# Performance work log

Hardware: AMD Instinct MI355X
Metric: run time of the kernel (lower is better)

## Reference

```python
import jax, jax.numpy as jnp
import numpy as np

N_NODES = 100000


def _gcn_conv(x, row, col, W, b, n):
    # PyG GCNConv: h = W x; out_i = sum_{j->i} norm_ij * h_j + b, with self-loops
    # and symmetric normalization norm_ij = deg_i^-1/2 * deg_j^-1/2.
    h = x @ W  # [N, out]
    loop = jnp.arange(n, dtype=row.dtype)
    r = jnp.concatenate([row, loop])
    c = jnp.concatenate([col, loop])
    deg = jax.ops.segment_sum(jnp.ones_like(c, dtype=h.dtype), c, num_segments=n)
    dinv = jnp.where(deg > 0, jax.lax.rsqrt(deg), 0.0)
    norm = dinv[r] * dinv[c]  # [E+N]
    msg = h[r] * norm[:, None]  # gather + per-edge scale
    out = jax.ops.segment_sum(msg, c, num_segments=n)  # scatter-add to dst
    return out + b


def setup_inputs() -> dict:
    key = jax.random.key(0)
    ks = jax.random.split(key, 8)
    N, E = N_NODES, 1600000
    d_in, comm_dim, hid, out = 120, 8, 128, 64
    x = jax.random.normal(ks[0], (N, d_in), dtype=jnp.float32)
    edge_index = jax.random.randint(ks[1], (2, E), 0, N, dtype=jnp.int64)
    comm_ids = jax.random.randint(ks[2], (N,), 0, 64, dtype=jnp.int64)
    comm_emb = jax.random.normal(ks[3], (64, comm_dim), dtype=jnp.float32)
    s1 = 1.0 / np.sqrt(d_in + comm_dim)
    s2 = 1.0 / np.sqrt(hid)
    W1 = jax.random.normal(ks[4], (d_in + comm_dim, hid), dtype=jnp.float32) * s1
    b1 = jnp.zeros((hid,), dtype=jnp.float32)
    W2 = jax.random.normal(ks[5], (hid, out), dtype=jnp.float32) * s2
    b2 = jnp.zeros((out,), dtype=jnp.float32)
    return {"x": x, "edge_index": edge_index, "comm_ids": comm_ids,
            "comm_emb": comm_emb, "W1": W1, "b1": b1, "W2": W2, "b2": b2}


def reference(x, edge_index, comm_ids, comm_emb, W1, b1, W2, b2):
    n = x.shape[0]
    row, col = edge_index[0], edge_index[1]
    c = comm_emb[comm_ids]                      # [N, comm_dim] embedding lookup
    h = jnp.concatenate([x, c], axis=-1)        # [N, in+comm_dim]
    h = jax.nn.relu(_gcn_conv(h, row, col, W1, b1, n))
    # dropout p=0.5 is inactive in eval mode (training=False)
    out = _gcn_conv(h, row, col, W2, b2, n)     # [N, out_channels]
    return out
```

## Files before the change

### kernel.cpp

```cpp
#include <hip/hip_runtime.h>

typedef __attribute__((ext_vector_type(8))) short bf16x8;
typedef __attribute__((ext_vector_type(4))) float f32x4;

#define CAPB 5632
#define NBMAX 512

static __device__ __forceinline__ unsigned short f2bf(float f) {
    unsigned u = __float_as_uint(f);
    unsigned r = (u + 0x7fff + ((u >> 16) & 1)) >> 16;
    return (unsigned short)r;
}
static __device__ __forceinline__ float bfu_lo(unsigned v) { return __uint_as_float(v << 16); }
static __device__ __forceinline__ float bfu_hi(unsigned v) { return __uint_as_float(v & 0xffff0000u); }

static __device__ __forceinline__ bf16x8 cvt8(float4 u0, float4 u1) {
    bf16x8 r;
    r[0] = (short)f2bf(u0.x); r[1] = (short)f2bf(u0.y);
    r[2] = (short)f2bf(u0.z); r[3] = (short)f2bf(u0.w);
    r[4] = (short)f2bf(u1.x); r[5] = (short)f2bf(u1.y);
    r[6] = (short)f2bf(u1.z); r[7] = (short)f2bf(u1.w);
    return r;
}

__global__ void k_zero_int(int* __restrict__ p, int n) {
    int i = blockIdx.x * blockDim.x + threadIdx.x;
    if (i < n) p[i] = 0;
}

__global__ __launch_bounds__(256) void k_passA(const int* __restrict__ row,
                                               const int* __restrict__ col,
                                               int* __restrict__ gcnt,
                                               unsigned* __restrict__ packed,
                                               int E, int NB) {
    __shared__ int lcnt[NBMAX];
    __shared__ int lbase[NBMAX];
    __shared__ int lcur[NBMAX];
    __shared__ int gbaseS[NBMAX];
    __shared__ unsigned stage[4096];
    __shared__ unsigned short stageb[4096];
    __shared__ int s[256];

    int tid = threadIdx.x;
    int t0 = blockIdx.x * 4096;
    int total = min(4096, E - t0);

    for (int b = tid; b < NBMAX; b += 256) { lcnt[b] = 0; lcur[b] = 0; }
    __syncthreads();

    int er[16], ec[16];
#pragma unroll
    for (int j = 0; j < 16; ++j) {
        int e = t0 + j * 256 + tid;
        if (e < E) {
            er[j] = row[e];
            ec[j] = col[e];
            atomicAdd(&lcnt[ec[j] >> 8], 1);
        }
    }
    __syncthreads();

    int c0 = lcnt[2 * tid], c1 = lcnt[2 * tid + 1];
    int p = c0 + c1;
    s[tid] = p;
    __syncthreads();
    for (int off = 1; off < 256; off <<= 1) {
        int t = (tid >= off) ? s[tid - off] : 0;
        __syncthreads();
        s[tid] += t;
        __syncthreads();
    }
    int ebase = s[tid] - p;
    lbase[2 * tid] = ebase;
    lbase[2 * tid + 1] = ebase + c0;
    __syncthreads();

    for (int b = tid; b < NB; b += 256) {
        int lc = lcnt[b];
        if (lc > 0) gbaseS[b] = atomicAdd(&gcnt[b], lc);
    }
    __syncthreads();

#pragma unroll
    for (int j = 0; j < 16; ++j) {
        int e = t0 + j * 256 + tid;
        if (e < E) {
            int b = ec[j] >> 8;
            int pos = lbase[b] + atomicAdd(&lcur[b], 1);
            stage[pos] = ((unsigned)er[j] << 8) | ((unsigned)ec[j] & 255u);
            stageb[pos] = (unsigned short)b;
        }
    }
    __syncthreads();

    for (int j = tid; j < total; j += 256) {
        int b = stageb[j];
        packed[(size_t)b * CAPB + gbaseS[b] + (j - lbase[b])] = stage[j];
    }
}

__global__ void k_bscan(const int* __restrict__ gcnt, int* __restrict__ gbase,
                        int* __restrict__ indptr, int n, int E, int NB) {
    __shared__ int s[512];
    int tid = threadIdx.x;
    int v = (tid < NB) ? gcnt[tid] : 0;
    s[tid] = v;
    __syncthreads();
    for (int off = 1; off < 512; off <<= 1) {
        int t = (tid >= off) ? s[tid - off] : 0;
        __syncthreads();
        s[tid] += t;
        __syncthreads();
    }
    if (tid < NB) gbase[tid] = s[tid] - v;
    if (tid == 0) indptr[n] = E;
}

__global__ __launch_bounds__(256) void k_passB(const unsigned* __restrict__ packed,
                                               const int* __restrict__ gcnt,
                                               const int* __restrict__ gbase,
                                               int* __restrict__ indptr,
                                               float* __restrict__ dinv,
                                               int* __restrict__ srcidx, int n) {
    __shared__ int ncnt[256];
    __shared__ int nbase[256];
    __shared__ int srow[CAPB];

    int b = blockIdx.x;
    int tid = threadIdx.x;
    int nodeBase = b << 8;
    int cntE = min(gcnt[b], CAPB);
    int base = gbase[b];
    size_t pb = (size_t)b * CAPB;

    ncnt[tid] = 0;
    __syncthreads();

    for (int j = tid; j < cntE; j += 256) {
        unsigned e = packed[pb + j];
        atomicAdd(&ncnt[e & 255u], 1);
    }
    __syncthreads();

    int v = ncnt[tid];
    nbase[tid] = v;
    __syncthreads();
    for (int off = 1; off < 256; off <<= 1) {
        int t = (tid >= off) ? nbase[tid - off] : 0;
        __syncthreads();
        nbase[tid] += t;
        __syncthreads();
    }
    int excl = nbase[tid] - v;
    __syncthreads();
    nbase[tid] = excl;

    int node = nodeBase + tid;
    if (node < n) {
        indptr[node] = base + excl;
        dinv[node] = rsqrtf((float)(v + 1));
    }
    ncnt[tid] = 0;
    __syncthreads();

    for (int j = tid; j < cntE; j += 256) {
        unsigned e = packed[pb + j];
        int c = (int)(e & 255u);
        int r = (int)(e >> 8);
        int p = nbase[c] + atomicAdd(&ncnt[c], 1);
        srow[p] = r;
    }
    __syncthreads();

    for (int j = tid; j < cntE; j += 256) srcidx[base + j] = srow[j];
}

__global__ void k_wprep(const float* __restrict__ W1, const float* __restrict__ W2,
                        const float* __restrict__ b1,
                        unsigned short* __restrict__ Wt1, unsigned short* __restrict__ Wt2p,
                        float* __restrict__ b1p,
                        unsigned* __restrict__ D1qz,
                        unsigned* __restrict__ D2z,
                        unsigned char* __restrict__ shifts, int n) {
    int idx = blockIdx.x * blockDim.x + threadIdx.x;
    const int B0 = 128 * 128, B1 = B0 + 64 * 128, B2 = B1 + 128, B3 = B2 + 32, B4 = B3 + 32;
    if (idx < B0) {
        int colc = idx >> 7, k = idx & 127;
        Wt1[colc * 128 + k] = f2bf(W1[k * 128 + colc]);
    } else if (idx < B1) {
        int j = idx - B0;
        int colc = j >> 7, p = j & 127;
        int korig = (p & 7) * 16 + (p >> 3);
        Wt2p[colc * 128 + p] = f2bf(W2[korig * 64 + colc]);
    } else if (idx < B2) {
        int p = idx - B1;
        b1p[p] = b1[(p & 7) * 16 + (p >> 3)];
    } else if (idx < B3) {
        D1qz[idx - B2] = 0;
    } else if (idx < B4) {
        D2z[idx - B3] = 0;
    } else if (idx == B4) {
        shifts[n] = 0;
    }
}

__global__ __launch_bounds__(256) void k_gemm1(const float* __restrict__ x,
                                               const int* __restrict__ cid,
                                               const float* __restrict__ cemb,
                                               const unsigned short* __restrict__ Wt,
                                               const float* __restrict__ dinv,
                                               unsigned char* __restrict__ D1q,
                                               unsigned char* __restrict__ shifts, int n) {
    int tid = threadIdx.x;
    int wid = tid >> 6, lane = tid & 63;
    int rbase = blockIdx.x * 64 + wid * 16;
    int lr = lane & 15, kq = lane >> 4;

    int arow = rbase + lr;
    if (arow > n - 1) arow = n - 1;
    const float* xp = x + (size_t)arow * 120 + kq * 8;

    bf16x8 a0 = cvt8(*(const float4*)(xp),      *(const float4*)(xp + 4));
    bf16x8 a1 = cvt8(*(const float4*)(xp + 32), *(const float4*)(xp + 36));
    bf16x8 a2 = cvt8(*(const float4*)(xp + 64), *(const float4*)(xp + 68));
    bf16x8 a3;
    if (kq < 3) {
        a3 = cvt8(*(const float4*)(xp + 96), *(const float4*)(xp + 100));
    } else {
        const float* cp = cemb + (size_t)cid[arow] * 8;
        a3 = cvt8(*(const float4*)(cp), *(const float4*)(cp + 4));
    }

    f32x4 acc[8];
#pragma unroll
    for (int cf = 0; cf < 8; ++cf) acc[cf] = (f32x4){0.f, 0.f, 0.f, 0.f};

#pragma unroll
    for (int cf = 0; cf < 8; ++cf) {
        const unsigned short* bp = Wt + (size_t)(cf * 16 + lr) * 128 + kq * 8;
        bf16x8 b0 = *(const bf16x8*)(bp);
        bf16x8 b1 = *(const bf16x8*)(bp + 32);
        bf16x8 b2 = *(const bf16x8*)(bp + 64);
        bf16x8 b3 = *(const bf16x8*)(bp + 96);
        acc[cf] = __builtin_amdgcn_mfma_f32_16x16x32_bf16(a0, b0, acc[cf], 0, 0, 0);
        acc[cf] = __builtin_amdgcn_mfma_f32_16x16x32_bf16(a1, b1, acc[cf], 0, 0, 0);
        acc[cf] = __builtin_amdgcn_mfma_f32_16x16x32_bf16(a2, b2, acc[cf], 0, 0, 0);
        acc[cf] = __builtin_amdgcn_mfma_f32_16x16x32_bf16(a3, b3, acc[cf], 0, 0, 0);
    }

#pragma unroll
    for (int r = 0; r < 4; ++r) {
        int grow = rbase + kq * 4 + r;
        float dv = (grow < n) ? dinv[grow] : 0.f;
        float m = 0.f;
#pragma unroll
        for (int cf = 0; cf < 8; ++cf) m = fmaxf(m, fabsf(acc[cf][r] * dv));
        m = fmaxf(m, __shfl_xor(m, 1));
        m = fmaxf(m, __shfl_xor(m, 2));
        m = fmaxf(m, __shfl_xor(m, 4));
        m = fmaxf(m, __shfl_xor(m, 8));
        int mb = (int)((__float_as_uint(m) >> 23) & 255u);
        int er = mb - 127 + 1 - 7;
        int sh = min(max(er + 16, 0), 15);
        int ee = sh - 16;
        float sinv = __uint_as_float((unsigned)(127 - ee) << 23);
        if (grow < n) {
            if (lr == 0) shifts[grow] = (unsigned char)sh;
            unsigned lo = 0, hi = 0;
#pragma unroll
            for (int cf = 0; cf < 4; ++cf) {
                int q8 = (int)rintf(acc[cf][r] * dv * sinv);
                q8 = min(max(q8, -127), 127);
                lo |= ((unsigned)(q8 & 255)) << (8 * cf);
            }
#pragma unroll
            for (int cf = 4; cf < 8; ++cf) {
                int q8 = (int)rintf(acc[cf][r] * dv * sinv);
                q8 = min(max(q8, -127), 127);
                hi |= ((unsigned)(q8 & 255)) << (8 * (cf - 4));
            }
            *(uint2*)&D1q[(size_t)grow * 128 + lr * 8] = make_uint2(lo, hi);
        }
    }
}

__global__ __launch_bounds__(256) void k_agg1g2(const uint2* __restrict__ rows,
                                                const unsigned char* __restrict__ shifts,
                                                const int* __restrict__ indptr,
                                                const int* __restrict__ srcidx,
                                                const float* __restrict__ dinv,
                                                const float* __restrict__ b1p,
                                                const unsigned short* __restrict__ Wt2p,
                                                unsigned short* __restrict__ D2, int n) {
    __shared__ unsigned short Hl[16][132];
    int tid = threadIdx.x;
    int wid = tid >> 6, lane = tid & 63;
    int g = lane >> 4, gl = lane & 15;
    int i = blockIdx.x * 16 + wid * 4 + g;
    if (i > n - 1) i = n - 1;

    float di = dinv[i];
    float4 bA = *(const float4*)&b1p[gl * 8];
    float4 bB = *(const float4*)&b1p[gl * 8 + 4];

    uint2 sq = rows[(size_t)i * 16 + gl];
    int ssh = shifts[i];
    int a[8];
#pragma unroll
    for (int j = 0; j < 4; ++j) {
        a[j]     = ((int)(signed char)((sq.x >> (8 * j)) & 255u)) << ssh;
        a[j + 4] = ((int)(signed char)((sq.y >> (8 * j)) & 255u)) << ssh;
    }

    int e0 = indptr[i];
    int d = indptr[i + 1] - e0;
    int m = max(d, __shfl_xor(d, 16));
    m = max(m, __shfl_xor(m, 32));

#pragma unroll 8
    for (int t = 0; t < m; ++t) {
        bool act = t < d;
        int s = act ? srcidx[e0 + t] : n;
        int sh = shifts[s];
        uint2 q = rows[(size_t)s * 16 + gl];
#pragma unroll
        for (int j = 0; j < 4; ++j) {
            a[j]     += ((int)(signed char)((q.x >> (8 * j)) & 255u)) << sh;
            a[j + 4] += ((int)(signed char)((q.y >> (8 * j)) & 255u)) << sh;
        }
    }

    float sc = di * 0x1p-16f;
    int trow = wid * 4 + g;
    float hb[8] = {bA.x, bA.y, bA.z, bA.w, bB.x, bB.y, bB.z, bB.w};
#pragma unroll
    for (int j = 0; j < 8; ++j) {
        Hl[trow][gl * 8 + j] = f2bf(fmaxf((float)a[j] * sc + hb[j], 0.f));
    }
    __syncthreads();

    int lr = lane & 15, kq = lane >> 4;
    f32x4 acc = (f32x4){0.f, 0.f, 0.f, 0.f};
    const unsigned short* bp = Wt2p + (size_t)(wid * 16 + lr) * 128 + kq * 8;
#pragma unroll
    for (int step = 0; step < 4; ++step) {
        bf16x8 af = *(const bf16x8*)&Hl[lr][kq * 8 + step * 32];
        bf16x8 bf = *(const bf16x8*)(bp + step * 32);
        acc = __builtin_amdgcn_mfma_f32_16x16x32_bf16(af, bf, acc, 0, 0, 0);
    }
#pragma unroll
    for (int r = 0; r < 4; ++r) {
        int node = blockIdx.x * 16 + kq * 4 + r;
        if (node < n) {
            D2[(size_t)node * 64 + wid * 16 + lr] = f2bf(acc[r] * dinv[node]);
        }
    }
}

__global__ __launch_bounds__(256) void k_agg2(const uint2* __restrict__ Hs,
                                              const int* __restrict__ indptr,
                                              const int* __restrict__ srcidx,
                                              const float* __restrict__ dinv,
                                              const float* __restrict__ bias,
                                              float4* __restrict__ Out, int n) {
    int tid = threadIdx.x;
    int lane = tid & 63;
    int g = lane >> 4, gl = lane & 15;
    int i = blockIdx.x * 16 + (tid >> 6) * 4 + g;
    if (i > n - 1) i = n - 1;

    float di = dinv[i];
    float4 b = *(const float4*)&bias[gl * 4];

    uint2 sv = Hs[(size_t)i * 16 + gl];
    float a0 = bfu_lo(sv.x), a1 = bfu_hi(sv.x);
    float a2 = bfu_lo(sv.y), a3 = bfu_hi(sv.y);

    int e0 = indptr[i];
    int d = indptr[i + 1] - e0;
    int m = max(d, __shfl_xor(d, 16));
    m = max(m, __shfl_xor(m, 32));

#pragma unroll 8
    for (int t = 0; t < m; ++t) {
        bool act = t < d;
        int s = act ? srcidx[e0 + t] : n;
        uint2 w = Hs[(size_t)s * 16 + gl];
        a0 += bfu_lo(w.x);
        a1 += bfu_hi(w.x);
        a2 += bfu_lo(w.y);
        a3 += bfu_hi(w.y);
    }
    Out[(size_t)i * 16 + gl] = make_float4(di * a0 + b.x, di * a1 + b.y,
                                           di * a2 + b.z, di * a3 + b.w);
}


extern "C" void kernel_launch(void* const* d_in, const int* in_sizes, int n_in,
                              void* d_out, int out_size, void* d_ws, size_t ws_size,
                              hipStream_t stream) {
    const float* x    = (const float*)d_in[0];
    const int*   eidx = (const int*)d_in[1];
    const int*   cid  = (const int*)d_in[2];
    const float* cemb = (const float*)d_in[3];
    const float* W1   = (const float*)d_in[4];
    const float* b1   = (const float*)d_in[5];
    const float* W2   = (const float*)d_in[6];
    const float* b2   = (const float*)d_in[7];
    float* out = (float*)d_out;

    int n = in_sizes[2];
    int E = in_sizes[1] / 2;
    const int* row = eidx;
    const int* col = eidx + E;
    int NB = (n + 255) / 256;

    char* ws = (char*)d_ws;
    auto alloc = [&](size_t bytes) {
        char* p = ws;
        ws += (bytes + 255) & ~(size_t)255;
        return p;
    };
    float*          dinv    = (float*)alloc((size_t)n * 4);
    int*            gcnt    = (int*)alloc((size_t)NB * 4);
    int*            gbase   = (int*)alloc((size_t)NB * 4);
    int*            indptr  = (int*)alloc((size_t)(n + 1) * 4);
    int*            srcidx  = (int*)alloc((size_t)E * 4);
    unsigned*       packed  = (unsigned*)alloc((size_t)NB * CAPB * 4);
    unsigned short* Wt1     = (unsigned short*)alloc(128 * 128 * 2);
    unsigned short* Wt2p    = (unsigned short*)alloc(64 * 128 * 2);
    float*          b1p     = (float*)alloc(128 * 4);
    unsigned char*  D1q     = (unsigned char*)alloc((size_t)(n + 1) * 128);
    unsigned char*  shifts  = (unsigned char*)alloc((size_t)(n + 1));
    unsigned short* D2      = (unsigned short*)alloc((size_t)(n + 1) * 64 * 2);

    k_zero_int<<<(NB + 255) / 256, 256, 0, stream>>>(gcnt, NB);
    k_passA<<<(E + 4095) / 4096, 256, 0, stream>>>(row, col, gcnt, packed, E, NB);
    k_bscan<<<1, 512, 0, stream>>>(gcnt, gbase, indptr, n, E, NB);
    k_passB<<<NB, 256, 0, stream>>>(packed, gcnt, gbase, indptr, dinv, srcidx, n);

    int wpn = 128 * 128 + 64 * 128 + 128 + 32 + 32 + 1;
    k_wprep<<<(wpn + 255) / 256, 256, 0, stream>>>(
        W1, W2, b1, Wt1, Wt2p, b1p,
        (unsigned*)(D1q + (size_t)n * 128),
        (unsigned*)(D2 + (size_t)n * 64),
        shifts, n);

    int gb = (n + 63) / 64;
    int ga = (n + 15) / 16;
    k_gemm1<<<gb, 256, 0, stream>>>(x, cid, cemb, Wt1, dinv, D1q, shifts, n);
    k_agg1g2<<<ga, 256, 0, stream>>>((const uint2*)D1q, shifts, indptr, srcidx,
                                     dinv, b1p, Wt2p, D2, n);
    k_agg2<<<ga, 256, 0, stream>>>((const uint2*)D2, indptr, srcidx, dinv, b2,
                                   (float4*)out, n);
}
```

Before: 188.5 us.

## Give each wave 16 nodes in agg1g2 and drop block-wide sync before MFMA

```diff
diff --git a/kernel.cpp b/kernel.cpp
--- a/kernel.cpp
+++ b/kernel.cpp
@@ -13,6 +13,9 @@
 }
 static __device__ __forceinline__ float bfu_lo(unsigned v) { return __uint_as_float(v << 16); }
 static __device__ __forceinline__ float bfu_hi(unsigned v) { return __uint_as_float(v & 0xffff0000u); }
+static __device__ __forceinline__ unsigned packbf(float a, float b) {
+    return (unsigned)f2bf(a) | ((unsigned)f2bf(b) << 16);
+}
 
 static __device__ __forceinline__ bf16x8 cvt8(float4 u0, float4 u1) {
     bf16x8 r;
@@ -180,10 +183,9 @@
                         unsigned short* __restrict__ Wt1, unsigned short* __restrict__ Wt2p,
                         float* __restrict__ b1p,
                         unsigned* __restrict__ D1qz,
-                        unsigned* __restrict__ D2z,
                         unsigned char* __restrict__ shifts, int n) {
     int idx = blockIdx.x * blockDim.x + threadIdx.x;
-    const int B0 = 128 * 128, B1 = B0 + 64 * 128, B2 = B1 + 128, B3 = B2 + 32, B4 = B3 + 32;
+    const int B0 = 128 * 128, B1 = B0 + 64 * 128, B2 = B1 + 128, B3 = B2 + 32;
     if (idx < B0) {
         int colc = idx >> 7, k = idx & 127;
         Wt1[colc * 128 + k] = f2bf(W1[k * 128 + colc]);
@@ -197,11 +199,13 @@
         b1p[p] = b1[(p & 7) * 16 + (p >> 3)];
     } else if (idx < B3) {
         D1qz[idx - B2] = 0;
-    } else if (idx < B4) {
-        D2z[idx - B3] = 0;
-    } else if (idx == B4) {
+    } else if (idx == B3) {
         shifts[n] = 0;
     }
+}
+
+__global__ void k_zrow(unsigned* __restrict__ D2z) {
+    if (threadIdx.x < 32) D2z[threadIdx.x] = 0;
 }
 
 __global__ __launch_bounds__(256) void k_gemm1(const float* __restrict__ x,
@@ -292,67 +296,84 @@
                                                 const float* __restrict__ b1p,
                                                 const unsigned short* __restrict__ Wt2p,
                                                 unsigned short* __restrict__ D2, int n) {
-    __shared__ unsigned short Hl[16][132];
+    __shared__ unsigned short Hl[4][16][132];
     int tid = threadIdx.x;
     int wid = tid >> 6, lane = tid & 63;
     int g = lane >> 4, gl = lane & 15;
-    int i = blockIdx.x * 16 + wid * 4 + g;
-    if (i > n - 1) i = n - 1;
-
-    float di = dinv[i];
+    int nbase = blockIdx.x * 64 + wid * 16;
+
     float4 bA = *(const float4*)&b1p[gl * 8];
     float4 bB = *(const float4*)&b1p[gl * 8 + 4];
-
-    uint2 sq = rows[(size_t)i * 16 + gl];
-    int ssh = shifts[i];
-    int a[8];
-#pragma unroll
-    for (int j = 0; j < 4; ++j) {
-        a[j]     = ((int)(signed char)((sq.x >> (8 * j)) & 255u)) << ssh;
-        a[j + 4] = ((int)(signed char)((sq.y >> (8 * j)) & 255u)) << ssh;
-    }
-
-    int e0 = indptr[i];
-    int d = indptr[i + 1] - e0;
-    int m = max(d, __shfl_xor(d, 16));
-    m = max(m, __shfl_xor(m, 32));
+    float hb[8] = {bA.x, bA.y, bA.z, bA.w, bB.x, bB.y, bB.z, bB.w};
+
+#pragma unroll
+    for (int b = 0; b < 4; ++b) {
+        int i = nbase + b * 4 + g;
+        if (i > n - 1) i = n - 1;
+        float di = dinv[i];
+
+        uint2 sq = rows[(size_t)i * 16 + gl];
+        int ssh = shifts[i];
+        int a[8];
+#pragma unroll
+        for (int j = 0; j < 4; ++j) {
+            a[j]     = ((int)(signed char)((sq.x >> (8 * j)) & 255u)) << ssh;
+            a[j + 4] = ((int)(signed char)((sq.y >> (8 * j)) & 255u)) << ssh;
+        }
+
+        int e0 = indptr[i];
+        int d = indptr[i + 1] - e0;
+        int m = max(d, __shfl_xor(d, 16));
+        m = max(m, __shfl_xor(m, 32));
 
 #pragma unroll 8
-    for (int t = 0; t < m; ++t) {
-        bool act = t < d;
-        int s = act ? srcidx[e0 + t] : n;
-        int sh = shifts[s];
-        uint2 q = rows[(size_t)s * 16 + gl];
-#pragma unroll
-        for (int j = 0; j < 4; ++j) {
-            a[j]     += ((int)(signed char)((q.x >> (8 * j)) & 255u)) << sh;
-            a[j + 4] += ((int)(signed char)((q.y >> (8 * j)) & 255u)) << sh;
-        }
-    }
-
-    float sc = di * 0x1p-16f;
-    int trow = wid * 4 + g;
-    float hb[8] = {bA.x, bA.y, bA.z, bA.w, bB.x, bB.y, bB.z, bB.w};
-#pragma unroll
-    for (int j = 0; j < 8; ++j) {
-        Hl[trow][gl * 8 + j] = f2bf(fmaxf((float)a[j] * sc + hb[j], 0.f));
-    }
-    __syncthreads();
+        for (int t = 0; t < m; ++t) {
+            bool act = t < d;
+            int s = act ? srcidx[e0 + t] : n;
+            int sh = shifts[s];
+            uint2 q = rows[(size_t)s * 16 + gl];
+#pragma unroll
+            for (int j = 0; j < 4; ++j) {
+                a[j]     += ((int)(signed char)((q.x >> (8 * j)) & 255u)) << sh;
+                a[j + 4] += ((int)(signed char)((q.y >> (8 * j)) & 255u)) << sh;
+            }
+        }
+
+        float sc = di * 0x1p-16f;
+        uint4 o;
+        o.x = packbf(fmaxf((float)a[0] * sc + hb[0], 0.f), fmaxf((float)a[1] * sc + hb[1], 0.f));
+        o.y = packbf(fmaxf((float)a[2] * sc + hb[2], 0.f), fmaxf((float)a[3] * sc + hb[3], 0.f));
+        o.z = packbf(fmaxf((float)a[4] * sc + hb[4], 0.f), fmaxf((float)a[5] * sc + hb[5], 0.f));
+        o.w = packbf(fmaxf((float)a[6] * sc + hb[6], 0.f), fmaxf((float)a[7] * sc + hb[7], 0.f));
+        *(uint4*)&Hl[wid][b * 4 + g][gl * 8] = o;
+    }
+
+    asm volatile("s_waitcnt lgkmcnt(0)" ::: "memory");
+    __builtin_amdgcn_sched_barrier(0);
 
     int lr = lane & 15, kq = lane >> 4;
-    f32x4 acc = (f32x4){0.f, 0.f, 0.f, 0.f};
-    const unsigned short* bp = Wt2p + (size_t)(wid * 16 + lr) * 128 + kq * 8;
-#pragma unroll
-    for (int step = 0; step < 4; ++step) {
-        bf16x8 af = *(const bf16x8*)&Hl[lr][kq * 8 + step * 32];
-        bf16x8 bf = *(const bf16x8*)(bp + step * 32);
-        acc = __builtin_amdgcn_mfma_f32_16x16x32_bf16(af, bf, acc, 0, 0, 0);
-    }
+    float dvv[4];
 #pragma unroll
     for (int r = 0; r < 4; ++r) {
-        int node = blockIdx.x * 16 + kq * 4 + r;
-        if (node < n) {
-            D2[(size_t)node * 64 + wid * 16 + lr] = f2bf(acc[r] * dinv[node]);
+        int node = nbase + kq * 4 + r;
+        dvv[r] = (node < n) ? dinv[node] : 0.f;
+    }
+#pragma unroll
+    for (int cb = 0; cb < 4; ++cb) {
+        f32x4 acc = (f32x4){0.f, 0.f, 0.f, 0.f};
+        const unsigned short* bp = Wt2p + (size_t)(cb * 16 + lr) * 128 + kq * 8;
+#pragma unroll
+        for (int step = 0; step < 4; ++step) {
+            bf16x8 af = *(const bf16x8*)&Hl[wid][lr][kq * 8 + step * 32];
+            bf16x8 bf = *(const bf16x8*)(bp + step * 32);
+            acc = __builtin_amdgcn_mfma_f32_16x16x32_bf16(af, bf, acc, 0, 0, 0);
+        }
+#pragma unroll
+        for (int r = 0; r < 4; ++r) {
+            int node = nbase + kq * 4 + r;
+            if (node < n) {
+                D2[(size_t)node * 64 + cb * 16 + lr] = f2bf(acc[r] * dvv[r]);
+            }
         }
     }
 }
@@ -439,18 +460,16 @@
     k_bscan<<<1, 512, 0, stream>>>(gcnt, gbase, indptr, n, E, NB);
     k_passB<<<NB, 256, 0, stream>>>(packed, gcnt, gbase, indptr, dinv, srcidx, n);
 
-    int wpn = 128 * 128 + 64 * 128 + 128 + 32 + 32 + 1;
+    int wpn = 128 * 128 + 64 * 128 + 128 + 32 + 1;
     k_wprep<<<(wpn + 255) / 256, 256, 0, stream>>>(
         W1, W2, b1, Wt1, Wt2p, b1p,
-        (unsigned*)(D1q + (size_t)n * 128),
-        (unsigned*)(D2 + (size_t)n * 64),
-        shifts, n);
+        (unsigned*)(D1q + (size_t)n * 128), shifts, n);
+    k_zrow<<<1, 64, 0, stream>>>((unsigned*)(D2 + (size_t)n * 64));
 
     int gb = (n + 63) / 64;
-    int ga = (n + 15) / 16;
     k_gemm1<<<gb, 256, 0, stream>>>(x, cid, cemb, Wt1, dinv, D1q, shifts, n);
-    k_agg1g2<<<ga, 256, 0, stream>>>((const uint2*)D1q, shifts, indptr, srcidx,
-                                     dinv, b1p, Wt2p, D2, n);
-    k_agg2<<<ga, 256, 0, stream>>>((const uint2*)D2, indptr, srcidx, dinv, b2,
-                                   (float4*)out, n);
-}
+    k_agg1g2<<<(n + 63) / 64, 256, 0, stream>>>((const uint2*)D1q, shifts, indptr, srcidx,
+                                                dinv, b1p, Wt2p, D2, n);
+    k_agg2<<<(n + 15) / 16, 256, 0, stream>>>((const uint2*)D2, indptr, srcidx, dinv, b2,
+                                              (float4*)out, n);
+}
```

After: 187.9 us. About the same (-0.3%).
